# Optimization experiments

Measured on AMD Instinct MI355X. Metric: run time of the kernel, lower is better.

Reference implementation:

```python
import jax, jax.numpy as jnp
import numpy as np

NEG_SLOPE = 0.2
N, E, NNZ, IN, H, C = 100000, 50000, 800000, 128, 8, 16


def setup_inputs() -> dict:
    key = jax.random.key(0)
    ks = jax.random.split(key, 8)
    X = jax.random.normal(ks[0], (N, IN), jnp.float32)
    W_typed = jax.random.normal(ks[1], (4, IN, H * C), jnp.float32) * (1.0 / np.sqrt(IN))
    att_e = jax.random.normal(ks[2], (4, H, C), jnp.float32) * 0.1
    att_v = jax.random.normal(ks[3], (4, H, C), jnp.float32) * 0.1
    vertex = jax.random.randint(ks[4], (NNZ,), 0, N, jnp.int32)
    edges = jax.random.randint(ks[5], (NNZ,), 0, E, jnp.int32)
    vtype = jax.random.randint(ks[6], (N,), 0, 4, jnp.int32)
    etype = jax.random.randint(ks[7], (E,), 0, 4, jnp.int32)
    return {"X": X, "W_typed": W_typed, "att_e": att_e, "att_v": att_v,
            "vertex": vertex, "edges": edges, "vtype": vtype, "etype": etype}


def _segment_softmax(logits, seg, num):
    # numerically-stable softmax over segments (PyG-style, eps in denominator)
    m = jax.ops.segment_max(logits, seg, num_segments=num)
    ex = jnp.exp(logits - m[seg])
    s = jax.ops.segment_sum(ex, seg, num_segments=num)
    return ex / (s[seg] + 1e-16)


def reference(X, W_typed, att_e, att_v, vertex, edges, vtype, etype):
    # typed linear: project with all 4 type weights, select per node type
    Xall = jnp.einsum('ni,tio->tno', X, W_typed)        # [4, N, H*C]
    X0 = Xall[vtype, jnp.arange(N)]                     # [N, H*C]
    Xn = X0.reshape(N, H, C)
    Xve = Xn[vertex]                                    # [NNZ, H, C] gather vertex->incidence
    # vertex->edge attention, typed by edge type of each incidence
    beta = jnp.sum(Xve * att_e[etype[edges]], axis=-1)  # [NNZ, H]
    beta = jax.nn.leaky_relu(beta, NEG_SLOPE)
    beta = _segment_softmax(beta, edges, E)
    Xe = jax.nn.relu(jax.ops.segment_sum(Xve * beta[..., None], edges, num_segments=E))  # [E, H, C]
    Xe = Xe[edges]                                      # [NNZ, H, C] gather edge->incidence
    # edge->vertex attention, typed by node type of each incidence's vertex
    alpha = jnp.sum(Xe * att_v[vtype[vertex]], axis=-1)  # [NNZ, H]
    alpha = jax.nn.leaky_relu(alpha, NEG_SLOPE)
    alpha = _segment_softmax(alpha, vertex, N)
    Xv = jax.ops.segment_sum(Xe * alpha[..., None], vertex, num_segments=N)  # [N, H, C]
    return Xv.reshape(N, H * C)
```

## Files before the change

### kernel.cpp

```cpp
#include <hip/hip_runtime.h>

typedef __attribute__((ext_vector_type(8))) short bf16x8;
typedef __attribute__((ext_vector_type(4))) float f32x4;

#define NEG_SLOPE 0.2f

__device__ __forceinline__ unsigned short f2bf(float f){
  unsigned u = __float_as_uint(f);
  u = (u + 0x7fffu + ((u >> 16) & 1u)) >> 16;
  return (unsigned short)u;
}
__device__ __forceinline__ float bflo(unsigned u){ return __uint_as_float(u << 16); }
__device__ __forceinline__ float bfhi(unsigned u){ return __uint_as_float(u & 0xffff0000u); }

__global__ __launch_bounds__(256) void k_histprep(
    const int* __restrict__ edges, const int* __restrict__ vertex, int NNZ,
    int* __restrict__ cnt, int E, int nbHist,
    const int* __restrict__ vtype, int N, int* __restrict__ tcnt, int nbHN,
    const float* __restrict__ W, short* __restrict__ Bfrag){
  __shared__ int lcnt[4];
  int b = (int)blockIdx.x;
  if (b < nbHist){
    int i = b * 256 + threadIdx.x;
    if (i < NNZ){
      atomicAdd(cnt + edges[i], 1);
      atomicAdd(cnt + E + vertex[i], 1);
    }
    return;
  }
  b -= nbHist;
  if (b < nbHN){
    if (threadIdx.x < 4) lcnt[threadIdx.x] = 0;
    __syncthreads();
    int i = b * 256 + threadIdx.x;
    if (i < N) atomicAdd(&lcnt[vtype[i]], 1);
    __syncthreads();
    if (threadIdx.x < 4 && lcnt[threadIdx.x] > 0)
      atomicAdd(tcnt + threadIdx.x, lcnt[threadIdx.x]);
    return;
  }
  b -= nbHN;
  int u = b * 256 + threadIdx.x;
  int j = u & 7, lane = (u >> 3) & 63, ct = (u >> 9) & 31, ks = u >> 14;
  int k = ks * 32 + ((lane >> 4) << 3) + j;
  int col = (ct << 4) + (lane & 15);
  int t = col >> 7, o = col & 127;
  Bfrag[u] = (short)f2bf(W[(t * 128 + k) * 128 + o]);
}

__global__ __launch_bounds__(256) void k_scanA(const int* __restrict__ cnt, int S,
                                               int* __restrict__ bsum){
  __shared__ int sh[256];
  int base = blockIdx.x * 1024 + threadIdx.x * 4;
  int s = 0;
  #pragma unroll
  for (int k = 0; k < 4; ++k){ int idx = base + k; if (idx < S) s += cnt[idx]; }
  sh[threadIdx.x] = s; __syncthreads();
  for (int off = 128; off > 0; off >>= 1){
    if (threadIdx.x < off) sh[threadIdx.x] += sh[threadIdx.x + off];
    __syncthreads();
  }
  if (threadIdx.x == 0) bsum[blockIdx.x] = sh[0];
}

__global__ void k_scanB(int* bsum, int nb, const int* __restrict__ tcnt,
                        int* __restrict__ pbase){
  if (threadIdx.x == 0 && blockIdx.x == 0){
    int run = 0;
    for (int b = 0; b < nb; ++b){ int v = bsum[b]; bsum[b] = run; run += v; }
    int pb = 0;
    for (int t = 0; t < 4; ++t){
      pbase[t] = pb;
      pb += ((tcnt[t] + 63) >> 6) << 6;
    }
    pbase[4] = pb;
  }
}

__global__ __launch_bounds__(256) void k_scanC(const int* __restrict__ cnt, int S,
    const int* __restrict__ bsum, int* __restrict__ offs, int* __restrict__ cursor,
    int nbS, const int* __restrict__ vtype, int N, const int* __restrict__ pbase,
    int* __restrict__ tcur, int* __restrict__ nsorted){
  __shared__ int sh[256];
  __shared__ int gbase[4];
  int t = threadIdx.x;
  int b = (int)blockIdx.x;
  if (b >= nbS){
    int* lcnt = sh;
    if (t < 4) lcnt[t] = 0;
    __syncthreads();
    int i = (b - nbS) * 256 + t;
    int tt = 0, rank = 0;
    bool valid = i < N;
    if (valid){ tt = vtype[i]; rank = atomicAdd(&lcnt[tt], 1); }
    __syncthreads();
    if (t < 4 && lcnt[t] > 0) gbase[t] = atomicAdd(tcur + t, lcnt[t]);
    __syncthreads();
    if (valid) nsorted[pbase[tt] + gbase[tt] + rank] = i;
    return;
  }
  int base = b * 1024 + t * 4;
  int c[4]; int s = 0;
  #pragma unroll
  for (int k = 0; k < 4; ++k){ int idx = base + k; c[k] = (idx < S) ? cnt[idx] : 0; s += c[k]; }
  sh[t] = s; __syncthreads();
  for (int off = 1; off < 256; off <<= 1){
    int v = (t >= off) ? sh[t - off] : 0; __syncthreads();
    sh[t] += v; __syncthreads();
  }
  int run = bsum[b] + sh[t] - s;
  #pragma unroll
  for (int k = 0; k < 4; ++k){
    int idx = base + k;
    if (idx < S){ offs[idx] = run; cursor[idx] = run; run += c[k]; }
  }
}

__global__ __launch_bounds__(256, 3) void k_gemm_place(const float* __restrict__ X,
    const short* __restrict__ Bfrag, const int* __restrict__ nsorted,
    const int* __restrict__ pbase, unsigned short* __restrict__ X0,
    const int* __restrict__ edges, const int* __restrict__ vertex, int NNZ,
    int* __restrict__ cursor, int* __restrict__ rows, int nbPlace){
  __shared__ short shB[8 * 4 * 64 * 8];
  const int tid = threadIdx.x;
  const int q = (int)blockIdx.x / 3, r = (int)blockIdx.x % 3;

  if (r != 0){
    int hb = 2 * q + (r - 1);
    if (hb < nbPlace){
      int i = hb * 256 + tid;
      if (i < NNZ){
        int pos = atomicAdd(cursor + edges[i], 1);
        rows[pos] = vertex[i];
      }
    }
    return;
  }

  const int rowIdx = q * 64;
  const int t = (rowIdx >= pbase[1]) + (rowIdx >= pbase[2]) + (rowIdx >= pbase[3]);

  const bf16x8* Bv = (const bf16x8*)Bfrag;
  bf16x8* shBv = (bf16x8*)shB;
  #pragma unroll
  for (int v = 0; v < 8; ++v){
    int item = v * 256 + tid;
    int slab = item >> 6, ln = item & 63;
    int ks = slab >> 3, ctl = slab & 7;
    shBv[item] = Bv[((ks * 32 + 8 * t + ctl) * 64) + ln];
  }

  const int w = tid >> 6, lane = tid & 63;
  const int m = lane & 15, qq = lane >> 4;
  const int node = nsorted[rowIdx + w * 16 + m];

  bf16x8 afrag[4];
  #pragma unroll
  for (int ks = 0; ks < 4; ++ks){
    bf16x8 f;
    if (node >= 0){
      const float4* src = (const float4*)(X + (size_t)node * 128 + ks * 32 + qq * 8);
      float4 a = src[0], b = src[1];
      f[0]=(short)f2bf(a.x); f[1]=(short)f2bf(a.y); f[2]=(short)f2bf(a.z); f[3]=(short)f2bf(a.w);
      f[4]=(short)f2bf(b.x); f[5]=(short)f2bf(b.y); f[6]=(short)f2bf(b.z); f[7]=(short)f2bf(b.w);
    } else {
      #pragma unroll
      for (int z = 0; z < 8; ++z) f[z] = 0;
    }
    afrag[ks] = f;
  }

  f32x4 acc[8];
  #pragma unroll
  for (int ct = 0; ct < 8; ++ct){
    acc[ct][0]=0.f; acc[ct][1]=0.f; acc[ct][2]=0.f; acc[ct][3]=0.f;
  }

  __syncthreads();
  #pragma unroll
  for (int ctl = 0; ctl < 8; ++ctl){
    #pragma unroll
    for (int ks = 0; ks < 4; ++ks){
      bf16x8 bf = shBv[(ks * 8 + ctl) * 64 + lane];
      acc[ctl] = __builtin_amdgcn_mfma_f32_16x16x32_bf16(afrag[ks], bf, acc[ctl], 0, 0, 0);
    }
  }

  const int col0 = lane & 15;
  #pragma unroll
  for (int rr = 0; rr < 4; ++rr){
    int row = nsorted[rowIdx + w * 16 + qq * 4 + rr];
    if (row < 0) continue;
    #pragma unroll
    for (int ctl = 0; ctl < 8; ++ctl)
      X0[(size_t)row * 128 + ctl * 16 + col0] = f2bf(acc[ctl][rr]);
  }
}

template<int OUT_BF16, int DO_RELU>
__device__ __forceinline__ void seg_body(const unsigned* __restrict__ feat,
    const float* __restrict__ att, const int* __restrict__ rows_sorted,
    const int* __restrict__ offs, const int* __restrict__ cnt,
    const int* __restrict__ stype, void* __restrict__ outbuf,
    int S, int blockId, int tid){
  int wid = tid >> 6, lane = tid & 63;
  int s = blockId * 4 + wid;
  if (s >= S) return;
  int t = stype[s];
  float a0 = att[t * 128 + 2 * lane], a1 = att[t * 128 + 2 * lane + 1];
  int start = offs[s], len = cnt[s];
  float denom = 0.f, acc0 = 0.f, acc1 = 0.f;

  for (int base = 0; base < len; base += 64){
    int m = len - base; if (m > 64) m = 64;
    int idx = 0;
    if (lane < m) idx = rows_sorted[start + base + lane];

    unsigned u0 = 0, u1 = 0, u2 = 0, u3 = 0;
    {
      int r;
      r = __shfl(idx, 0); if (0 < m) u0 = feat[(size_t)r * 64 + lane];
      r = __shfl(idx, 1); if (1 < m) u1 = feat[(size_t)r * 64 + lane];
      r = __shfl(idx, 2); if (2 < m) u2 = feat[(size_t)r * 64 + lane];
      r = __shfl(idx, 3); if (3 < m) u3 = feat[(size_t)r * 64 + lane];
    }
    for (int j = 0; j < m; j += 2){
      unsigned ua = u0, ub = u1;
      u0 = u2; u1 = u3;
      if (j + 4 < m){ int rn = __shfl(idx, j + 4); u2 = feat[(size_t)rn * 64 + lane]; }
      if (j + 5 < m){ int rn = __shfl(idx, j + 5); u3 = feat[(size_t)rn * 64 + lane]; }

      float xa0 = bflo(ua), xa1 = bfhi(ua);
      float xb0 = bflo(ub), xb1 = bfhi(ub);
      float pa = xa0 * a0 + xa1 * a1;
      float pb = xb0 * a0 + xb1 * a1;
      pa += __shfl_xor(pa, 1);  pb += __shfl_xor(pb, 1);
      pa += __shfl_xor(pa, 2);  pb += __shfl_xor(pb, 2);
      pa += __shfl_xor(pa, 4);  pb += __shfl_xor(pb, 4);
      pa = pa > 0.f ? pa : NEG_SLOPE * pa;
      float wa = __expf(pa);
      denom += wa; acc0 += wa * xa0; acc1 += wa * xa1;
      if (j + 1 < m){
        pb = pb > 0.f ? pb : NEG_SLOPE * pb;
        float wb = __expf(pb);
        denom += wb; acc0 += wb * xb0; acc1 += wb * xb1;
      }
    }
  }
  float inv = 1.f / (denom + 1e-16f);
  float v0 = acc0 * inv, v1 = acc1 * inv;
  if (DO_RELU){ v0 = fmaxf(v0, 0.f); v1 = fmaxf(v1, 0.f); }
  if (OUT_BF16){
    unsigned pw = (unsigned)f2bf(v0) | ((unsigned)f2bf(v1) << 16);
    ((unsigned*)outbuf)[(size_t)s * 64 + lane] = pw;
  } else {
    ((float2*)outbuf)[(size_t)s * 64 + lane] = make_float2(v0, v1);
  }
}

__global__ __launch_bounds__(256) void k_place_seg1(
    const int* __restrict__ edges, const int* __restrict__ vertex, int NNZ,
    int* __restrict__ cursor, int* __restrict__ rows, int E,
    int nbPlace, int nbSeg,
    const unsigned* __restrict__ X0, const float* __restrict__ att_e,
    const int* __restrict__ offs, const int* __restrict__ cnt,
    const int* __restrict__ etype, void* __restrict__ Xe){
  const int q = (int)blockIdx.x / 5, r = (int)blockIdx.x % 5;
  if (r == 0){
    if (q < nbPlace){
      int i = q * 256 + threadIdx.x;
      if (i < NNZ){
        int pos = atomicAdd(cursor + E + vertex[i], 1);
        rows[pos] = edges[i];
      }
    }
    return;
  }
  int segBlk = q * 4 + (r - 1);
  if (segBlk >= nbSeg) return;
  seg_body<1, 1>(X0, att_e, rows, offs, cnt, etype, Xe, E, segBlk, threadIdx.x);
}

__global__ __launch_bounds__(256) void k_seg2(const unsigned* __restrict__ Xe,
    const float* __restrict__ att_v, const int* __restrict__ rows,
    const int* __restrict__ offs, const int* __restrict__ cnt,
    const int* __restrict__ vtype, float* __restrict__ out, int N){
  seg_body<0, 0>(Xe, att_v, rows, offs, cnt, vtype, out, N,
                 (int)blockIdx.x, threadIdx.x);
}

extern "C" void kernel_launch(void* const* d_in, const int* in_sizes, int n_in,
                              void* d_out, int out_size, void* d_ws, size_t ws_size,
                              hipStream_t stream){
  const float* X      = (const float*)d_in[0];
  const float* W      = (const float*)d_in[1];
  const float* att_e  = (const float*)d_in[2];
  const float* att_v  = (const float*)d_in[3];
  const int*   vertex = (const int*)d_in[4];
  const int*   edges  = (const int*)d_in[5];
  const int*   vtype  = (const int*)d_in[6];
  const int*   etype  = (const int*)d_in[7];
  float* out = (float*)d_out;
  const int N   = in_sizes[0] / 128;
  const int NNZ = in_sizes[4];
  const int E   = in_sizes[7];
  const int S   = E + N;

  const int nbI = (NNZ + 255) / 256;
  const int nbHN = (N + 255) / 256;
  const int nbS = (S + 1023) / 1024;
  const int nbSeg1 = (E + 3) / 4;
  const int nbPad = (N + 252 + 63) / 64;
  const int nsortedCap = nbPad * 64;

  char* wp = (char*)d_ws;
  int* cnt    = (int*)wp; wp += (size_t)S * 4;
  int* tcnt   = (int*)wp; wp += 16;
  int* tcur   = (int*)wp; wp += 16;
  int* offs   = (int*)wp; wp += (size_t)S * 4;
  int* cursor = (int*)wp; wp += (size_t)S * 4;
  int* bsum   = (int*)wp; wp += 1024;
  int* pbase  = (int*)wp; wp += 32;
  int* rows   = (int*)wp; wp += (size_t)2 * NNZ * 4;
  int* nsorted= (int*)wp; wp += (size_t)nsortedCap * 4;
  unsigned short* X0 = (unsigned short*)wp; wp += (size_t)N * 128 * 2;
  unsigned short* Xe = (unsigned short*)wp; wp += (size_t)E * 128 * 2;
  short* Bfrag = (short*)wp; wp += (size_t)65536 * 2;

  hipMemsetAsync(cnt, 0, (size_t)(S + 8) * 4, stream);
  hipMemsetAsync(nsorted, 0xFF, (size_t)nsortedCap * 4, stream);

  k_histprep<<<nbI + nbHN + 256, 256, 0, stream>>>(edges, vertex, NNZ, cnt, E,
      nbI, vtype, N, tcnt, nbHN, W, Bfrag);

  k_scanA<<<nbS, 256, 0, stream>>>(cnt, S, bsum);
  k_scanB<<<1, 64, 0, stream>>>(bsum, nbS, tcnt, pbase);
  k_scanC<<<nbS + nbHN, 256, 0, stream>>>(cnt, S, bsum, offs, cursor,
      nbS, vtype, N, pbase, tcur, nsorted);

  k_gemm_place<<<3 * nbPad, 256, 0, stream>>>(X, Bfrag, nsorted, pbase,
      (unsigned short*)X0, edges, vertex, NNZ, cursor, rows, nbI);

  k_place_seg1<<<5 * nbI, 256, 0, stream>>>(edges, vertex, NNZ, cursor,
      rows, E, nbI, nbSeg1, (const unsigned*)X0, att_e, offs, cnt, etype, Xe);

  k_seg2<<<(N + 3) / 4, 256, 0, stream>>>((const unsigned*)Xe, att_v,
      rows, offs + E, cnt + E, vtype, out, N);
}
```

Measured before the change: 364.3 us.

## Process four rows per wave with 16-byte loads in segment softmax

Reworks the segment attention body so each 16-lane quarter of a wave handles a different incidence row. Each lane loads 8 bf16 features with a uint4 load, and the quarters are reduced across the wave at the end. The goal is more memory-level parallelism and fewer shuffle reductions per row, since the head dot product now needs only one xor shuffle. The cost is higher register use for eight accumulators, a final cross-quarter reduction, and only one quarter of the lanes doing the stores.

```diff
diff --git a/kernel.cpp b/kernel.cpp
--- a/kernel.cpp
+++ b/kernel.cpp
@@ -12,6 +12,7 @@
 }
 __device__ __forceinline__ float bflo(unsigned u){ return __uint_as_float(u << 16); }
 __device__ __forceinline__ float bfhi(unsigned u){ return __uint_as_float(u & 0xffff0000u); }
+__device__ __forceinline__ float lrelu(float x){ return x > 0.f ? x : NEG_SLOPE * x; }
 
 __global__ __launch_bounds__(256) void k_histprep(
     const int* __restrict__ edges, const int* __restrict__ vertex, int NNZ,
@@ -197,8 +198,8 @@
   }
 }
 
-template<int OUT_BF16, int DO_RELU>
-__device__ __forceinline__ void seg_body(const unsigned* __restrict__ feat,
+template<int OUT_BF16>
+__device__ __forceinline__ void seg_body(const uint4* __restrict__ feat,
     const float* __restrict__ att, const int* __restrict__ rows_sorted,
     const int* __restrict__ offs, const int* __restrict__ cnt,
     const int* __restrict__ stype, void* __restrict__ outbuf,
@@ -207,54 +208,89 @@
   int s = blockId * 4 + wid;
   if (s >= S) return;
   int t = stype[s];
-  float a0 = att[t * 128 + 2 * lane], a1 = att[t * 128 + 2 * lane + 1];
+  int sub = lane >> 4, lane16 = lane & 15;
+  const float4* ap = (const float4*)(att + t * 128 + lane16 * 8);
+  float4 A0 = ap[0], A1 = ap[1];
   int start = offs[s], len = cnt[s];
-  float denom = 0.f, acc0 = 0.f, acc1 = 0.f;
+  float denom = 0.f;
+  float acc[8];
+  #pragma unroll
+  for (int e = 0; e < 8; ++e) acc[e] = 0.f;
 
   for (int base = 0; base < len; base += 64){
     int m = len - base; if (m > 64) m = 64;
     int idx = 0;
     if (lane < m) idx = rows_sorted[start + base + lane];
-
-    unsigned u0 = 0, u1 = 0, u2 = 0, u3 = 0;
+    int ng = (m + 3) >> 2;
+    uint4 uA = make_uint4(0,0,0,0), uB = make_uint4(0,0,0,0);
     {
-      int r;
-      r = __shfl(idx, 0); if (0 < m) u0 = feat[(size_t)r * 64 + lane];
-      r = __shfl(idx, 1); if (1 < m) u1 = feat[(size_t)r * 64 + lane];
-      r = __shfl(idx, 2); if (2 < m) u2 = feat[(size_t)r * 64 + lane];
-      r = __shfl(idx, 3); if (3 < m) u3 = feat[(size_t)r * 64 + lane];
-    }
-    for (int j = 0; j < m; j += 2){
-      unsigned ua = u0, ub = u1;
-      u0 = u2; u1 = u3;
-      if (j + 4 < m){ int rn = __shfl(idx, j + 4); u2 = feat[(size_t)rn * 64 + lane]; }
-      if (j + 5 < m){ int rn = __shfl(idx, j + 5); u3 = feat[(size_t)rn * 64 + lane]; }
-
-      float xa0 = bflo(ua), xa1 = bfhi(ua);
-      float xb0 = bflo(ub), xb1 = bfhi(ub);
-      float pa = xa0 * a0 + xa1 * a1;
-      float pb = xb0 * a0 + xb1 * a1;
-      pa += __shfl_xor(pa, 1);  pb += __shfl_xor(pb, 1);
-      pa += __shfl_xor(pa, 2);  pb += __shfl_xor(pb, 2);
-      pa += __shfl_xor(pa, 4);  pb += __shfl_xor(pb, 4);
-      pa = pa > 0.f ? pa : NEG_SLOPE * pa;
-      float wa = __expf(pa);
-      denom += wa; acc0 += wa * xa0; acc1 += wa * xa1;
-      if (j + 1 < m){
-        pb = pb > 0.f ? pb : NEG_SLOPE * pb;
-        float wb = __expf(pb);
-        denom += wb; acc0 += wb * xb0; acc1 += wb * xb1;
+      int r0 = __shfl(idx, sub);
+      if (sub < m) uA = feat[(size_t)r0 * 16 + lane16];
+      int r1 = __shfl(idx, 4 + sub);
+      if (4 + sub < m) uB = feat[(size_t)r1 * 16 + lane16];
+    }
+    for (int g = 0; g < ng; g += 2){
+      {
+        uint4 u = uA;
+        int nr = (g + 2) * 4 + sub;
+        int rn = __shfl(idx, nr & 63);
+        if (nr < m) uA = feat[(size_t)rn * 16 + lane16];
+        float x0 = bflo(u.x), x1 = bfhi(u.x), x2 = bflo(u.y), x3 = bfhi(u.y);
+        float x4 = bflo(u.z), x5 = bfhi(u.z), x6 = bflo(u.w), x7 = bfhi(u.w);
+        float p = x0*A0.x + x1*A0.y + x2*A0.z + x3*A0.w
+                + x4*A1.x + x5*A1.y + x6*A1.z + x7*A1.w;
+        p += __shfl_xor(p, 1);
+        float wgt = __expf(lrelu(p));
+        wgt = (g * 4 + sub < m) ? wgt : 0.f;
+        denom += wgt;
+        acc[0] += wgt*x0; acc[1] += wgt*x1; acc[2] += wgt*x2; acc[3] += wgt*x3;
+        acc[4] += wgt*x4; acc[5] += wgt*x5; acc[6] += wgt*x6; acc[7] += wgt*x7;
       }
-    }
+      if (g + 1 < ng){
+        uint4 u = uB;
+        int nr = (g + 3) * 4 + sub;
+        int rn = __shfl(idx, nr & 63);
+        if (nr < m) uB = feat[(size_t)rn * 16 + lane16];
+        float x0 = bflo(u.x), x1 = bfhi(u.x), x2 = bflo(u.y), x3 = bfhi(u.y);
+        float x4 = bflo(u.z), x5 = bfhi(u.z), x6 = bflo(u.w), x7 = bfhi(u.w);
+        float p = x0*A0.x + x1*A0.y + x2*A0.z + x3*A0.w
+                + x4*A1.x + x5*A1.y + x6*A1.z + x7*A1.w;
+        p += __shfl_xor(p, 1);
+        float wgt = __expf(lrelu(p));
+        wgt = ((g + 1) * 4 + sub < m) ? wgt : 0.f;
+        denom += wgt;
+        acc[0] += wgt*x0; acc[1] += wgt*x1; acc[2] += wgt*x2; acc[3] += wgt*x3;
+        acc[4] += wgt*x4; acc[5] += wgt*x5; acc[6] += wgt*x6; acc[7] += wgt*x7;
+      }
+    }
+  }
+  denom += __shfl_xor(denom, 16);
+  denom += __shfl_xor(denom, 32);
+  #pragma unroll
+  for (int e = 0; e < 8; ++e){
+    acc[e] += __shfl_xor(acc[e], 16);
+    acc[e] += __shfl_xor(acc[e], 32);
   }
   float inv = 1.f / (denom + 1e-16f);
-  float v0 = acc0 * inv, v1 = acc1 * inv;
-  if (DO_RELU){ v0 = fmaxf(v0, 0.f); v1 = fmaxf(v1, 0.f); }
-  if (OUT_BF16){
-    unsigned pw = (unsigned)f2bf(v0) | ((unsigned)f2bf(v1) << 16);
-    ((unsigned*)outbuf)[(size_t)s * 64 + lane] = pw;
+  float v[8];
+  #pragma unroll
+  for (int e = 0; e < 8; ++e) v[e] = acc[e] * inv;
+
+  if constexpr (OUT_BF16){
+    if (sub == 0){
+      uint4 pw;
+      pw.x = (unsigned)f2bf(fmaxf(v[0],0.f)) | ((unsigned)f2bf(fmaxf(v[1],0.f)) << 16);
+      pw.y = (unsigned)f2bf(fmaxf(v[2],0.f)) | ((unsigned)f2bf(fmaxf(v[3],0.f)) << 16);
+      pw.z = (unsigned)f2bf(fmaxf(v[4],0.f)) | ((unsigned)f2bf(fmaxf(v[5],0.f)) << 16);
+      pw.w = (unsigned)f2bf(fmaxf(v[6],0.f)) | ((unsigned)f2bf(fmaxf(v[7],0.f)) << 16);
+      ((uint4*)outbuf)[(size_t)s * 16 + lane16] = pw;
+    }
   } else {
-    ((float2*)outbuf)[(size_t)s * 64 + lane] = make_float2(v0, v1);
+    if (sub == 0){
+      float4* op = (float4*)outbuf;
+      op[(size_t)s * 32 + lane16 * 2]     = make_float4(v[0], v[1], v[2], v[3]);
+      op[(size_t)s * 32 + lane16 * 2 + 1] = make_float4(v[4], v[5], v[6], v[7]);
+    }
   }
 }
 
@@ -262,7 +298,7 @@
     const int* __restrict__ edges, const int* __restrict__ vertex, int NNZ,
     int* __restrict__ cursor, int* __restrict__ rows, int E,
     int nbPlace, int nbSeg,
-    const unsigned* __restrict__ X0, const float* __restrict__ att_e,
+    const uint4* __restrict__ X0, const float* __restrict__ att_e,
     const int* __restrict__ offs, const int* __restrict__ cnt,
     const int* __restrict__ etype, void* __restrict__ Xe){
   const int q = (int)blockIdx.x / 5, r = (int)blockIdx.x % 5;
@@ -278,15 +314,15 @@
   }
   int segBlk = q * 4 + (r - 1);
   if (segBlk >= nbSeg) return;
-  seg_body<1, 1>(X0, att_e, rows, offs, cnt, etype, Xe, E, segBlk, threadIdx.x);
-}
-
-__global__ __launch_bounds__(256) void k_seg2(const unsigned* __restrict__ Xe,
+  seg_body<1>(X0, att_e, rows, offs, cnt, etype, Xe, E, segBlk, threadIdx.x);
+}
+
+__global__ __launch_bounds__(256) void k_seg2(const uint4* __restrict__ Xe,
     const float* __restrict__ att_v, const int* __restrict__ rows,
     const int* __restrict__ offs, const int* __restrict__ cnt,
     const int* __restrict__ vtype, float* __restrict__ out, int N){
-  seg_body<0, 0>(Xe, att_v, rows, offs, cnt, vtype, out, N,
-                 (int)blockIdx.x, threadIdx.x);
+  seg_body<0>(Xe, att_v, rows, offs, cnt, vtype, out, N,
+              (int)blockIdx.x, threadIdx.x);
 }
 
 extern "C" void kernel_launch(void* const* d_in, const int* in_sizes, int n_in,
@@ -342,8 +378,8 @@
       (unsigned short*)X0, edges, vertex, NNZ, cursor, rows, nbI);
 
   k_place_seg1<<<5 * nbI, 256, 0, stream>>>(edges, vertex, NNZ, cursor,
-      rows, E, nbI, nbSeg1, (const unsigned*)X0, att_e, offs, cnt, etype, Xe);
-
-  k_seg2<<<(N + 3) / 4, 256, 0, stream>>>((const unsigned*)Xe, att_v,
+      rows, E, nbI, nbSeg1, (const uint4*)X0, att_e, offs, cnt, etype, Xe);
+
+  k_seg2<<<(N + 3) / 4, 256, 0, stream>>>((const uint4*)Xe, att_v,
       rows, offs + E, cnt + E, vtype, out, N);
 }
```

Measured after the change: 346.5 us. -4.9%, faster.
